# Performance work log

Hardware: AMD Instinct MI355X
Metric: run time of the kernel (lower is better)

Reference implementation:

```python
import jax, jax.numpy as jnp
import numpy as np

N = 20000      # nodes per graph
E = 320000     # edges per graph (before self-loops)
G = 256        # graphs (strings) per side
VOCAB = 128    # NUMBER_EMBEDDINGS
D_IN = 128
HID = 64
H = 4
D_OUT = 128
NEG_SLOPE = 0.2  # PyG GATConv leaky_relu slope


def _gat(x, edge_index, W, att_s, att_d, bias, concat):
    """PyG GATConv: gather -> per-edge logits -> segment softmax over dst -> scatter.
    x: [N, F_in], W: [F_in, H*C], att_s/att_d: [H, C], bias: [H*C] or [C].
    Self-loops are added (PyG default add_self_loops=True)."""
    n = x.shape[0]
    h, c = att_s.shape
    loops = jnp.arange(n)
    src = jnp.concatenate([edge_index[0], loops])  # message sources j
    dst = jnp.concatenate([edge_index[1], loops])  # message targets i
    xh = (x @ W).reshape(n, h, c)                  # [N,H,C]
    a_s = jnp.einsum('nhc,hc->nh', xh, att_s)      # [N,H]
    a_d = jnp.einsum('nhc,hc->nh', xh, att_d)
    logits = jax.nn.leaky_relu(a_s[src] + a_d[dst], NEG_SLOPE)  # [E',H]
    m = jax.ops.segment_max(logits, dst, num_segments=n)
    m = jnp.where(jnp.isfinite(m), m, 0.0)
    e = jnp.exp(logits - m[dst])
    z = jax.ops.segment_sum(e, dst, num_segments=n)
    alpha = e / (z[dst] + 1e-16)                   # [E',H]
    msg = xh[src] * alpha[:, :, None]              # [E',H,C]
    out = jax.ops.segment_sum(msg, dst, num_segments=n)  # [N,H,C]
    out = out.reshape(n, h * c) if concat else out.mean(axis=1)
    return out + bias


def _encode(xi, ei, batch, emb, W1, as1, ad1, b1, lw1, lb1,
            W2, as2, ad2, b2, lw2, lb2, W3, as3, ad3, b3, lw3, lb3):
    e = emb[xi]  # [N, D_IN]
    x = jax.nn.relu(_gat(e, ei, W1, as1, ad1, b1, True) + e @ lw1 + lb1)
    x = jax.nn.relu(_gat(x, ei, W2, as2, ad2, b2, True) + x @ lw2 + lb2)
    x = _gat(x, ei, W3, as3, ad3, b3, False) + x @ lw3 + lb3  # [N, D_OUT]
    s = jax.ops.segment_sum(x, batch, num_segments=G)
    cnt = jax.ops.segment_sum(jnp.ones((x.shape[0],), x.dtype), batch, num_segments=G)
    return s / jnp.maximum(cnt, 1.0)[:, None]  # global_mean_pool -> [G, D_OUT]


def setup_inputs() -> dict:
    key = jax.random.key(0)
    ks = jax.random.split(key, 32)
    hc = H * HID  # 256
    def nrm(k, shape, scale=0.05):
        return jax.random.normal(k, shape, dtype=jnp.float32) * scale
    inp = {
        'x_l': jax.random.randint(ks[0], (N,), 0, VOCAB),
        'edge_l': jax.random.randint(ks[1], (2, E), 0, N),
        'batch_l': jnp.sort(jax.random.randint(ks[2], (N,), 0, G)),
        'x_r': jax.random.randint(ks[3], (N,), 0, VOCAB),
        'edge_r': jax.random.randint(ks[4], (2, E), 0, N),
        'batch_r': jnp.sort(jax.random.randint(ks[5], (N,), 0, G)),
        'emb': nrm(ks[6], (VOCAB, D_IN), 1.0),
        'W1': nrm(ks[7], (D_IN, hc)), 'as1': nrm(ks[8], (H, HID)), 'ad1': nrm(ks[9], (H, HID)),
        'b1': jnp.zeros((hc,), jnp.float32), 'lw1': nrm(ks[10], (D_IN, hc)), 'lb1': jnp.zeros((hc,), jnp.float32),
        'W2': nrm(ks[11], (hc, hc)), 'as2': nrm(ks[12], (H, HID)), 'ad2': nrm(ks[13], (H, HID)),
        'b2': jnp.zeros((hc,), jnp.float32), 'lw2': nrm(ks[14], (hc, hc)), 'lb2': jnp.zeros((hc,), jnp.float32),
        'W3': nrm(ks[15], (hc, H * D_OUT)), 'as3': nrm(ks[16], (H, D_OUT)), 'ad3': nrm(ks[17], (H, D_OUT)),
        'b3': jnp.zeros((D_OUT,), jnp.float32), 'lw3': nrm(ks[18], (hc, D_OUT)), 'lb3': jnp.zeros((D_OUT,), jnp.float32),
    }
    return inp


def reference(x_l, edge_l, batch_l, x_r, edge_r, batch_r, emb,
              W1, as1, ad1, b1, lw1, lb1,
              W2, as2, ad2, b2, lw2, lb2,
              W3, as3, ad3, b3, lw3, lb3):
    params = (emb, W1, as1, ad1, b1, lw1, lb1, W2, as2, ad2, b2, lw2, lb2,
              W3, as3, ad3, b3, lw3, lb3)
    out_l = _encode(x_l, edge_l, batch_l, *params)
    out_r = _encode(x_r, edge_r, batch_r, *params)
    return (out_l, out_r)
```

## Files before the change

kernel.cpp:

```cpp
#include <hip/hip_runtime.h>

#define GG 256

typedef __bf16 bf16x8 __attribute__((ext_vector_type(8)));
typedef __bf16 bf16x4 __attribute__((ext_vector_type(4)));
typedef float floatx4 __attribute__((ext_vector_type(4)));
typedef float f32x2 __attribute__((ext_vector_type(2)));

__device__ __forceinline__ float lrelu(float x) { return x > 0.f ? x : 0.2f * x; }

__device__ __forceinline__ int permM(int m) {
    int g = m >> 6, q = m & 63;
    return (g << 6) | ((q & 3) << 4) | (q >> 2);
}

__device__ __forceinline__ void wt1(const float* __restrict__ B, __bf16* __restrict__ Bt,
                                    int K, int M, int idx) {
    int k = idx / M, m = idx - k * M;
    Bt[(size_t)permM(m) * K + k] = (__bf16)B[idx];
}
__device__ __forceinline__ void wattn1(const float* __restrict__ W,
                                       const float* __restrict__ as_,
                                       const float* __restrict__ ad_,
                                       __bf16* __restrict__ dst, int K, int C, int idx) {
    int j = idx / K, k = idx - j * K;
    float v = 0.f;
    if (j < 8) {
        int h = j & 3;
        const float* att = (j < 4) ? as_ : ad_;
        int M = 4 * C;
        for (int c = 0; c < C; c++) v += W[(size_t)k * M + h * C + c] * att[h * C + c];
    }
    dst[(size_t)j * K + k] = (__bf16)v;
}

__global__ void k_wprep(const float* W1, const float* lw1, const float* as1, const float* ad1,
                        const float* W2, const float* lw2, const float* as2, const float* ad2,
                        const float* W3, const float* lw3, const float* as3, const float* ad3,
                        __bf16* B1t, __bf16* B2t, __bf16* B3t) {
    int idx = blockIdx.x * blockDim.x + threadIdx.x;
    if (idx < 32768) { wt1(W1, B1t, 128, 256, idx); return; }
    idx -= 32768;
    if (idx < 32768) { wt1(lw1, B1t + 256 * 128, 128, 256, idx); return; }
    idx -= 32768;
    if (idx < 2048) { wattn1(W1, as1, ad1, B1t + 512 * 128, 128, 64, idx); return; }
    idx -= 2048;
    if (idx < 65536) { wt1(W2, B2t, 256, 256, idx); return; }
    idx -= 65536;
    if (idx < 65536) { wt1(lw2, B2t + 256 * 256, 256, 256, idx); return; }
    idx -= 65536;
    if (idx < 4096) { wattn1(W2, as2, ad2, B2t + 512 * 256, 256, 64, idx); return; }
    idx -= 4096;
    if (idx < 131072) { wt1(W3, B3t, 256, 512, idx); return; }
    idx -= 131072;
    if (idx < 32768) { wt1(lw3, B3t + 512 * 256, 256, 128, idx); return; }
    idx -= 32768;
    if (idx < 4096) { wattn1(W3, as3, ad3, B3t + 640 * 256, 256, 128, idx); return; }
}

template <int K, bool EMB, bool LINBF>
__global__ __launch_bounds__(256) void k_gemm_all(const __bf16* __restrict__ A,
                                                  const int* __restrict__ xl,
                                                  const int* __restrict__ xr,
                                                  const float* __restrict__ emb,
                                                  const __bf16* __restrict__ Bt,
                                                  int n, int n1, int Mx, int Ml,
                                                  unsigned char* __restrict__ x8, int ldx,
                                                  float* __restrict__ linf,
                                                  __bf16* __restrict__ linb, int ldl,
                                                  const float* __restrict__ bias1,
                                                  const float* __restrict__ bias2,
                                                  float* __restrict__ a_s,
                                                  float* __restrict__ a_d) {
    constexpr int KS = K / 32;
    constexpr int LDK = K + 8;
    constexpr int LPR = K / 8;
    constexpr int NCH = 64 * LPR / 256;
    __shared__ __bf16 S[64 * LDK];
    int tid = threadIdx.x;
    int wave = tid >> 6, lane = tid & 63;
    int row0 = blockIdx.x * 64;
#pragma unroll
    for (int c = 0; c < NCH; c++) {
        int i = tid + c * 256;
        int r = i / LPR, ko = (i - r * LPR) * 8;
        int gr = row0 + r;
        bf16x8 v = {};
        if (gr < n) {
            if (EMB) {
                int xi = (gr < n1) ? xl[gr] : xr[gr - n1];
                const float4* src = (const float4*)(emb + ((size_t)xi << 7) + ko);
                float4 q0 = src[0], q1 = src[1];
                v = bf16x8{(__bf16)q0.x, (__bf16)q0.y, (__bf16)q0.z, (__bf16)q0.w,
                           (__bf16)q1.x, (__bf16)q1.y, (__bf16)q1.z, (__bf16)q1.w};
            } else {
                v = *(const bf16x8*)(A + (size_t)gr * K + ko);
            }
        }
        *(bf16x8*)&S[r * LDK + ko] = v;
    }
    __syncthreads();
    int kOff = (lane >> 4) * 8;
    int colBase = lane & 15;
    bf16x8 af[KS];
#pragma unroll
    for (int ks = 0; ks < KS; ks++)
        af[ks] = *(const bf16x8*)&S[(wave * 16 + colBase) * LDK + ks * 32 + kOff];
    int Mtot = Mx + Ml;
    int gr0 = row0 + wave * 16 + ((lane >> 4) << 2);
    int half = (Mtot / 128) * 64;
    int c0beg = blockIdx.y * half;
    int T = half / 64;
    bf16x8 regs[NCH];
#pragma unroll
    for (int c = 0; c < NCH; c++) {
        int i = tid + c * 256;
        int r = i / LPR, ko = (i - r * LPR) * 8;
        regs[c] = *(const bf16x8*)(Bt + (size_t)(c0beg + r) * K + ko);
    }
    for (int t = 0; t < T; t++) {
        __syncthreads();
#pragma unroll
        for (int c = 0; c < NCH; c++) {
            int i = tid + c * 256;
            int r = i / LPR, ko = (i - r * LPR) * 8;
            *(bf16x8*)&S[r * LDK + ko] = regs[c];
        }
        if (t + 1 < T) {
            int c0n = c0beg + (t + 1) * 64;
#pragma unroll
            for (int c = 0; c < NCH; c++) {
                int i = tid + c * 256;
                int r = i / LPR, ko = (i - r * LPR) * 8;
                regs[c] = *(const bf16x8*)(Bt + (size_t)(c0n + r) * K + ko);
            }
        }
        __syncthreads();
        floatx4 acc[4] = {};
#pragma unroll
        for (int ct = 0; ct < 4; ct++) {
#pragma unroll
            for (int ks = 0; ks < KS; ks++) {
                bf16x8 bf = *(const bf16x8*)&S[(ct * 16 + colBase) * LDK + ks * 32 + kOff];
                acc[ct] = __builtin_amdgcn_mfma_f32_16x16x32_bf16(af[ks], bf, acc[ct], 0, 0, 0);
            }
        }
        int c0 = c0beg + t * 64;
        if (c0 < Mx) {
#pragma unroll
            for (int r = 0; r < 4; r++) {
                int gr = gr0 + r;
                if (gr >= n) continue;
                int p = __builtin_amdgcn_cvt_pk_fp8_f32(acc[0][r], acc[1][r], 0, false);
                p = __builtin_amdgcn_cvt_pk_fp8_f32(acc[2][r], acc[3][r], p, true);
                *(unsigned int*)(x8 + (size_t)gr * ldx + c0 + colBase * 4) = (unsigned int)p;
            }
        } else {
            int c2 = c0 + colBase * 4 - Mx;
#pragma unroll
            for (int r = 0; r < 4; r++) {
                int gr = gr0 + r;
                if (gr >= n) continue;
                float v0 = acc[0][r] + bias1[c2 + 0];
                float v1 = acc[1][r] + bias1[c2 + 1];
                float v2 = acc[2][r] + bias1[c2 + 2];
                float v3 = acc[3][r] + bias1[c2 + 3];
                if (bias2) {
                    v0 += bias2[c2 + 0]; v1 += bias2[c2 + 1];
                    v2 += bias2[c2 + 2]; v3 += bias2[c2 + 3];
                }
                if (LINBF) {
                    bf16x4 o = {(__bf16)v0, (__bf16)v1, (__bf16)v2, (__bf16)v3};
                    *(bf16x4*)(linb + (size_t)gr * ldl + c2) = o;
                } else {
                    float4 o = {v0, v1, v2, v3};
                    *(float4*)(linf + (size_t)gr * ldl + c2) = o;
                }
            }
        }
    }
    if (blockIdx.y == 1) {
        floatx4 acc = {};
        const __bf16* bp = Bt + (size_t)(Mtot + colBase) * K + kOff;
#pragma unroll
        for (int ks = 0; ks < KS; ks++) {
            bf16x8 bf = *(const bf16x8*)(bp + ks * 32);
            acc = __builtin_amdgcn_mfma_f32_16x16x32_bf16(af[ks], bf, acc, 0, 0, 0);
        }
        if (colBase < 8) {
            float* dst = (colBase < 4) ? a_s : a_d;
            int h = colBase & 3;
#pragma unroll
            for (int r = 0; r < 4; r++) {
                int gr = gr0 + r;
                if (gr < n) dst[gr * 4 + h] = acc[r];
            }
        }
    }
}

__global__ void k_hist2(const int* __restrict__ el, const int* __restrict__ er,
                        int E, int n, int* __restrict__ deg) {
    int e = blockIdx.x * blockDim.x + threadIdx.x;
    if (e >= 2 * E) return;
    int d = (e < E) ? el[E + e] : er[E + (e - E)] + n;
    atomicAdd(&deg[d], 1);
}

__global__ __launch_bounds__(1024) void k_scan1(int* __restrict__ rp, int n,
                                                int* __restrict__ part) {
    __shared__ int wsum[16];
    int i = blockIdx.x * 1024 + threadIdx.x;
    int lane = threadIdx.x & 63, wid = threadIdx.x >> 6;
    int v = (i < n) ? rp[i] : 0;
    int inc = v;
#pragma unroll
    for (int off = 1; off < 64; off <<= 1) {
        int t = __shfl_up(inc, off, 64);
        if (lane >= off) inc += t;
    }
    if (lane == 63) wsum[wid] = inc;
    __syncthreads();
    if (wid == 0) {
        int wv = (lane < 16) ? wsum[lane] : 0;
        int winc = wv;
#pragma unroll
        for (int off = 1; off < 16; off <<= 1) {
            int t = __shfl_up(winc, off, 64);
            if (lane >= off) winc += t;
        }
        if (lane < 16) wsum[lane] = winc - wv;
        if (lane == 15) part[blockIdx.x] = winc;
    }
    __syncthreads();
    if (i < n) rp[i] = wsum[wid] + (inc - v);
}

__global__ void k_scan2(int* __restrict__ part, int nb) {
    int lane = threadIdx.x;
    int v = (lane < nb) ? part[lane] : 0;
    int inc = v;
#pragma unroll
    for (int off = 1; off < 64; off <<= 1) {
        int t = __shfl_up(inc, off, 64);
        if (lane >= off) inc += t;
    }
    if (lane < nb) part[lane] = inc - v;
}

__global__ __launch_bounds__(1024) void k_scan3(int* __restrict__ rp, int n,
                                                const int* __restrict__ part) {
    int i = blockIdx.x * 1024 + threadIdx.x;
    if (i < n) rp[i] += part[blockIdx.x];
}

__global__ void k_fill2(const int* __restrict__ el, const int* __restrict__ er,
                        int E, int n, int* __restrict__ rp, int* __restrict__ csr) {
    int e = blockIdx.x * blockDim.x + threadIdx.x;
    if (e >= 2 * E) return;
    int d, s;
    if (e < E) { s = el[e]; d = el[E + e]; }
    else       { s = er[e - E] + n; d = er[E + (e - E)] + n; }
    int pos = atomicAdd(&rp[d], 1);
    csr[pos] = s;
}

__device__ __forceinline__ void dec4(unsigned int u, float* f) {
    f32x2 a = __builtin_amdgcn_cvt_pk_f32_fp8(u, false);
    f32x2 b = __builtin_amdgcn_cvt_pk_f32_fp8(u, true);
    f[0] = a[0]; f[1] = a[1]; f[2] = b[0]; f[3] = b[1];
}

__global__ __launch_bounds__(256) void k_agg12(const int* __restrict__ rp,
                                               const int* __restrict__ csr,
                                               const float* __restrict__ a_s,
                                               const float* __restrict__ a_d,
                                               const unsigned char* __restrict__ x8,
                                               const __bf16* __restrict__ lin,
                                               __bf16* __restrict__ out_bf, int n) {
    int wv = (int)((blockIdx.x * blockDim.x + threadIdx.x) >> 6);
    int lane = threadIdx.x & 63;
    int sub = lane >> 5, sl = lane & 31;
    int node = wv * 2 + sub;
    if (node >= n) return;
    int c0 = sl * 8;
    int h = sl >> 3;
    int start = node ? rp[node - 1] : 0;
    int end = rp[node];
    float ad = a_d[node * 4 + h];
    float z = __expf(lrelu(a_s[node * 4 + h] + ad));
    float acc[8];
    {
        uint2 u = *(const uint2*)(x8 + (size_t)node * 256 + c0);
        float f[8];
        dec4(u.x, f); dec4(u.y, f + 4);
#pragma unroll
        for (int j = 0; j < 8; j++) acc[j] = z * f[j];
    }
    uint2 u0 = {}, u1 = {}, u2 = {};
    float A0 = 0.f, A1 = 0.f, A2 = 0.f;
    if (start < end) {
        int s = csr[start];
        u0 = *(const uint2*)(x8 + (size_t)s * 256 + c0);
        A0 = a_s[s * 4 + h];
    }
    if (start + 1 < end) {
        int s = csr[start + 1];
        u1 = *(const uint2*)(x8 + (size_t)s * 256 + c0);
        A1 = a_s[s * 4 + h];
    }
    if (start + 2 < end) {
        int s = csr[start + 2];
        u2 = *(const uint2*)(x8 + (size_t)s * 256 + c0);
        A2 = a_s[s * 4 + h];
    }
    for (int e = start; e < end; e++) {
        uint2 uc = u0;
        float ac = A0;
        u0 = u1; A0 = A1;
        u1 = u2; A1 = A2;
        if (e + 3 < end) {
            int s = csr[e + 3];
            u2 = *(const uint2*)(x8 + (size_t)s * 256 + c0);
            A2 = a_s[s * 4 + h];
        }
        float w = __expf(lrelu(ac + ad));
        z += w;
        float f[8];
        dec4(uc.x, f); dec4(uc.y, f + 4);
#pragma unroll
        for (int q = 0; q < 8; q++) acc[q] += w * f[q];
    }
    float inv = 1.f / (z + 1e-16f);
    bf16x8 l = *(const bf16x8*)(lin + (size_t)node * 256 + c0);
    bf16x8 r;
#pragma unroll
    for (int j = 0; j < 8; j++)
        r[j] = (__bf16)fmaxf(acc[j] * inv + (float)l[j], 0.f);
    *(bf16x8*)(out_bf + (size_t)node * 256 + c0) = r;
}

__global__ __launch_bounds__(256) void k_agg3(const int* __restrict__ rp,
                                              const int* __restrict__ csr,
                                              const float* __restrict__ a_s,
                                              const float* __restrict__ a_d,
                                              const unsigned int* __restrict__ x8,
                                              float* __restrict__ mean, int n) {
    int wv = (int)((blockIdx.x * blockDim.x + threadIdx.x) >> 6);
    int lane = threadIdx.x & 63;
    int sub = lane >> 5, sl = lane & 31;
    int node = wv * 2 + sub;
    if (node >= n) return;
    int h = sl >> 3;
    int start = node ? rp[node - 1] : 0;
    int end = rp[node];
    float ad = a_d[node * 4 + h];
    float z = __expf(lrelu(a_s[node * 4 + h] + ad));
    float acc[16];
    {
        uint4 u = *(const uint4*)(x8 + (size_t)node * 128 + sl * 4);
        float f[16];
        dec4(u.x, f); dec4(u.y, f + 4); dec4(u.z, f + 8); dec4(u.w, f + 12);
#pragma unroll
        for (int j = 0; j < 16; j++) acc[j] = z * f[j];
    }
    uint4 u0 = {}, u1 = {}, u2 = {};
    float A0 = 0.f, A1 = 0.f, A2 = 0.f;
    if (start < end) {
        int s = csr[start];
        u0 = *(const uint4*)(x8 + (size_t)s * 128 + sl * 4);
        A0 = a_s[s * 4 + h];
    }
    if (start + 1 < end) {
        int s = csr[start + 1];
        u1 = *(const uint4*)(x8 + (size_t)s * 128 + sl * 4);
        A1 = a_s[s * 4 + h];
    }
    if (start + 2 < end) {
        int s = csr[start + 2];
        u2 = *(const uint4*)(x8 + (size_t)s * 128 + sl * 4);
        A2 = a_s[s * 4 + h];
    }
    for (int e = start; e < end; e++) {
        uint4 uc = u0;
        float ac = A0;
        u0 = u1; A0 = A1;
        u1 = u2; A1 = A2;
        if (e + 3 < end) {
            int s = csr[e + 3];
            u2 = *(const uint4*)(x8 + (size_t)s * 128 + sl * 4);
            A2 = a_s[s * 4 + h];
        }
        float w = __expf(lrelu(ac + ad));
        z += w;
        float f[16];
        dec4(uc.x, f); dec4(uc.y, f + 4); dec4(uc.z, f + 8); dec4(uc.w, f + 12);
#pragma unroll
        for (int q = 0; q < 16; q++) acc[q] += w * f[q];
    }
    float scale = 0.25f / (z + 1e-16f);
#pragma unroll
    for (int j = 0; j < 16; j++) {
        float v = acc[j] * scale;
        v += __shfl_xor(v, 8, 64);
        v += __shfl_xor(v, 16, 64);
        acc[j] = v;
    }
    if ((sl & 24) == 0) {
        float4* op = (float4*)(mean + (size_t)node * 128 + sl * 16);
#pragma unroll
        for (int q = 0; q < 4; q++) {
            float4 o = {acc[4 * q], acc[4 * q + 1], acc[4 * q + 2], acc[4 * q + 3]};
            op[q] = o;
        }
    }
}

__global__ __launch_bounds__(128) void k_pool(const float* __restrict__ mean,
                                              const float* __restrict__ lin3,
                                              const float* __restrict__ b3,
                                              const int* __restrict__ bl,
                                              const int* __restrict__ br,
                                              int n, float* __restrict__ out) {
    int g = blockIdx.x, c = threadIdx.x;
    const int* b = (g < GG) ? bl : br;
    int tg = (g < GG) ? g : g - GG;
    int off = (g < GG) ? 0 : n;
    int s, e;
    { int lo = 0, hi = n; while (lo < hi) { int m = (lo + hi) >> 1; if (b[m] < tg) lo = m + 1; else hi = m; } s = lo; }
    { int lo = 0, hi = n; while (lo < hi) { int m = (lo + hi) >> 1; if (b[m] < tg + 1) lo = m + 1; else hi = m; } e = lo; }
    s += off; e += off;
    float acc = 0.f;
    for (int i = s; i < e; i++)
        acc += mean[(size_t)i * 128 + c] + lin3[(size_t)i * 128 + c];
    int cnt = e - s;
    out[(size_t)g * 128 + c] = cnt > 0 ? acc / (float)cnt + b3[c] : 0.f;
}

static inline int cdiv(int a, int b) { return (a + b - 1) / b; }

extern "C" void kernel_launch(void* const* d_in, const int* in_sizes, int n_in,
                              void* d_out, int out_size, void* d_ws, size_t ws_size,
                              hipStream_t stream) {
    const int* x_l = (const int*)d_in[0];
    const int* edge_l = (const int*)d_in[1];
    const int* batch_l = (const int*)d_in[2];
    const int* x_r = (const int*)d_in[3];
    const int* edge_r = (const int*)d_in[4];
    const int* batch_r = (const int*)d_in[5];
    const float* emb = (const float*)d_in[6];
    const float* W1 = (const float*)d_in[7];
    const float* as1 = (const float*)d_in[8];
    const float* ad1 = (const float*)d_in[9];
    const float* b1 = (const float*)d_in[10];
    const float* lw1 = (const float*)d_in[11];
    const float* lb1 = (const float*)d_in[12];
    const float* W2 = (const float*)d_in[13];
    const float* as2 = (const float*)d_in[14];
    const float* ad2 = (const float*)d_in[15];
    const float* b2 = (const float*)d_in[16];
    const float* lw2 = (const float*)d_in[17];
    const float* lb2 = (const float*)d_in[18];
    const float* W3 = (const float*)d_in[19];
    const float* as3 = (const float*)d_in[20];
    const float* ad3 = (const float*)d_in[21];
    const float* b3 = (const float*)d_in[22];
    const float* lw3 = (const float*)d_in[23];
    const float* lb3 = (const float*)d_in[24];

    const int n = in_sizes[0];
    const int E = in_sizes[1] / 2;
    const int N2 = 2 * n;
    const int NB = cdiv(N2, 1024);

    float* MEAN = (float*)d_ws;
    float* L3 = MEAN + (size_t)N2 * 128;
    float* a_s = L3 + (size_t)N2 * 128;
    float* a_d = a_s + (size_t)N2 * 4;
    int* rp = (int*)(a_d + (size_t)N2 * 4);
    int* csr = rp + N2;
    int* part = csr + 2 * E;
    __bf16* LINb = (__bf16*)(part + 64);
    unsigned char* X8a = (unsigned char*)(LINb + (size_t)N2 * 256);
    unsigned char* X8b = X8a + (size_t)N2 * 256;
    __bf16* Abf = (__bf16*)(X8b + (size_t)N2 * 512);
    __bf16* B1t = Abf + (size_t)N2 * 256;
    __bf16* B2t = B1t + 528 * 128;
    __bf16* B3t = B2t + 528 * 256;

    const int TB = 256;
    dim3 blk(TB);

    k_wprep<<<cdiv(370688, TB), blk, 0, stream>>>(W1, lw1, as1, ad1, W2, lw2, as2, ad2,
                                                  W3, lw3, as3, ad3, B1t, B2t, B3t);

    hipMemsetAsync(rp, 0, sizeof(int) * (size_t)N2, stream);
    k_hist2<<<cdiv(2 * E, TB), blk, 0, stream>>>(edge_l, edge_r, E, n, rp);
    k_scan1<<<NB, 1024, 0, stream>>>(rp, N2, part);
    k_scan2<<<1, 64, 0, stream>>>(part, NB);
    k_scan3<<<NB, 1024, 0, stream>>>(rp, N2, part);
    k_fill2<<<cdiv(2 * E, TB), blk, 0, stream>>>(edge_l, edge_r, E, n, rp, csr);

    k_gemm_all<128, true, true><<<dim3(cdiv(N2, 64), 2), blk, 0, stream>>>(
        nullptr, x_l, x_r, emb, B1t, N2, n, 256, 256, X8a, 256, nullptr, LINb, 256, lb1, b1, a_s, a_d);
    k_agg12<<<cdiv(N2, 8), blk, 0, stream>>>(rp, csr, a_s, a_d, X8a, LINb, Abf, N2);

    k_gemm_all<256, false, true><<<dim3(cdiv(N2, 64), 2), blk, 0, stream>>>(
        Abf, nullptr, nullptr, nullptr, B2t, N2, n, 256, 256, X8a, 256, nullptr, LINb, 256, lb2, b2, a_s, a_d);
    k_agg12<<<cdiv(N2, 8), blk, 0, stream>>>(rp, csr, a_s, a_d, X8a, LINb, Abf, N2);

    k_gemm_all<256, false, false><<<dim3(cdiv(N2, 64), 2), blk, 0, stream>>>(
        Abf, nullptr, nullptr, nullptr, B3t, N2, n, 512, 128, X8b, 512, L3, nullptr, 128, lb3, nullptr, a_s, a_d);
    k_agg3<<<cdiv(N2, 8), blk, 0, stream>>>(rp, csr, a_s, a_d, (const unsigned int*)X8b, MEAN, N2);
    k_pool<<<2 * GG, 128, 0, stream>>>(MEAN, L3, b3, batch_l, batch_r, n, (float*)d_out);
}
```

Measured before the change: 450.7 us.

## Reassociate layer-3 GEMM after aggregation and mean pooling

Layer 3 no longer runs a per-node 256x512 GEMM. The attention-weighted aggregation now works on the layer-2 output itself, stored as fp8 by agg12, and is pooled per graph into a small per-head buffer. The W3 and lw3 projections are then applied once per graph in a final small kernel. Attention logits come from a separate dot-product kernel. This cuts the large third GEMM and the wide x8 gather, at the cost of per-head accumulators (32 per lane), shared and global atomics, and extra fp8 quantization of the layer-2 activations.

Result: slower. 611.7 us (+35.7%).

```diff
diff --git a/kernel.cpp b/kernel.cpp
--- a/kernel.cpp
+++ b/kernel.cpp
@@ -37,7 +37,7 @@
 __global__ void k_wprep(const float* W1, const float* lw1, const float* as1, const float* ad1,
                         const float* W2, const float* lw2, const float* as2, const float* ad2,
                         const float* W3, const float* lw3, const float* as3, const float* ad3,
-                        __bf16* B1t, __bf16* B2t, __bf16* B3t) {
+                        __bf16* B1t, __bf16* B2t, __bf16* AT3, float* W3T, float* lw3T) {
     int idx = blockIdx.x * blockDim.x + threadIdx.x;
     if (idx < 32768) { wt1(W1, B1t, 128, 256, idx); return; }
     idx -= 32768;
@@ -51,11 +51,19 @@
     idx -= 65536;
     if (idx < 4096) { wattn1(W2, as2, ad2, B2t + 512 * 256, 256, 64, idx); return; }
     idx -= 4096;
-    if (idx < 131072) { wt1(W3, B3t, 256, 512, idx); return; }
+    if (idx < 131072) {
+        int m = idx >> 8, k = idx & 255;
+        W3T[(size_t)m * 256 + k] = W3[(size_t)k * 512 + m];
+        return;
+    }
     idx -= 131072;
-    if (idx < 32768) { wt1(lw3, B3t + 512 * 256, 256, 128, idx); return; }
+    if (idx < 32768) {
+        int c = idx >> 8, k = idx & 255;
+        lw3T[(size_t)c * 256 + k] = lw3[(size_t)k * 128 + c];
+        return;
+    }
     idx -= 32768;
-    if (idx < 4096) { wattn1(W3, as3, ad3, B3t + 640 * 256, 256, 128, idx); return; }
+    if (idx < 4096) { wattn1(W3, as3, ad3, AT3, 256, 128, idx); }
 }
 
 template <int K, bool EMB, bool LINBF>
@@ -271,13 +279,26 @@
     f[0] = a[0]; f[1] = a[1]; f[2] = b[0]; f[3] = b[1];
 }
 
+__global__ void k_cnt(const int* __restrict__ bl, const int* __restrict__ br,
+                      int n1, float* __restrict__ cinv) {
+    int g = threadIdx.x;
+    const int* b = (g < GG) ? bl : br;
+    int tg = (g < GG) ? g : g - GG;
+    int s, e;
+    { int lo = 0, hi = n1; while (lo < hi) { int m = (lo + hi) >> 1; if (b[m] < tg) lo = m + 1; else hi = m; } s = lo; }
+    { int lo = 0, hi = n1; while (lo < hi) { int m = (lo + hi) >> 1; if (b[m] < tg + 1) lo = m + 1; else hi = m; } e = lo; }
+    int cnt = e - s;
+    cinv[g] = cnt > 0 ? 1.f / (float)cnt : 0.f;
+}
+
 __global__ __launch_bounds__(256) void k_agg12(const int* __restrict__ rp,
                                                const int* __restrict__ csr,
                                                const float* __restrict__ a_s,
                                                const float* __restrict__ a_d,
                                                const unsigned char* __restrict__ x8,
                                                const __bf16* __restrict__ lin,
-                                               __bf16* __restrict__ out_bf, int n) {
+                                               __bf16* __restrict__ out_bf, int n,
+                                               unsigned char* __restrict__ x8o) {
     int wv = (int)((blockIdx.x * blockDim.x + threadIdx.x) >> 6);
     int lane = threadIdx.x & 63;
     int sub = lane >> 5, sl = lane & 31;
@@ -333,108 +354,223 @@
     }
     float inv = 1.f / (z + 1e-16f);
     bf16x8 l = *(const bf16x8*)(lin + (size_t)node * 256 + c0);
+    float rv[8];
+#pragma unroll
+    for (int j = 0; j < 8; j++)
+        rv[j] = fmaxf(acc[j] * inv + (float)l[j], 0.f);
     bf16x8 r;
 #pragma unroll
-    for (int j = 0; j < 8; j++)
-        r[j] = (__bf16)fmaxf(acc[j] * inv + (float)l[j], 0.f);
+    for (int j = 0; j < 8; j++) r[j] = (__bf16)rv[j];
     *(bf16x8*)(out_bf + (size_t)node * 256 + c0) = r;
-}
-
-__global__ __launch_bounds__(256) void k_agg3(const int* __restrict__ rp,
-                                              const int* __restrict__ csr,
-                                              const float* __restrict__ a_s,
-                                              const float* __restrict__ a_d,
-                                              const unsigned int* __restrict__ x8,
-                                              float* __restrict__ mean, int n) {
-    int wv = (int)((blockIdx.x * blockDim.x + threadIdx.x) >> 6);
-    int lane = threadIdx.x & 63;
-    int sub = lane >> 5, sl = lane & 31;
-    int node = wv * 2 + sub;
+    if (x8o) {
+        int p0 = __builtin_amdgcn_cvt_pk_fp8_f32(rv[0], rv[1], 0, false);
+        p0 = __builtin_amdgcn_cvt_pk_fp8_f32(rv[2], rv[3], p0, true);
+        int p1 = __builtin_amdgcn_cvt_pk_fp8_f32(rv[4], rv[5], 0, false);
+        p1 = __builtin_amdgcn_cvt_pk_fp8_f32(rv[6], rv[7], p1, true);
+        uint2 pv;
+        pv.x = (unsigned int)p0; pv.y = (unsigned int)p1;
+        *(uint2*)(x8o + (size_t)node * 256 + c0) = pv;
+    }
+}
+
+__global__ __launch_bounds__(256) void k_attn3(const __bf16* __restrict__ A,
+                                               const __bf16* __restrict__ T,
+                                               float* __restrict__ a_s,
+                                               float* __restrict__ a_d, int n) {
+    int idx = blockIdx.x * 256 + threadIdx.x;
+    int node = idx >> 3, j = idx & 7;
     if (node >= n) return;
-    int h = sl >> 3;
-    int start = node ? rp[node - 1] : 0;
-    int end = rp[node];
-    float ad = a_d[node * 4 + h];
-    float z = __expf(lrelu(a_s[node * 4 + h] + ad));
-    float acc[16];
-    {
-        uint4 u = *(const uint4*)(x8 + (size_t)node * 128 + sl * 4);
-        float f[16];
-        dec4(u.x, f); dec4(u.y, f + 4); dec4(u.z, f + 8); dec4(u.w, f + 12);
-#pragma unroll
-        for (int j = 0; j < 16; j++) acc[j] = z * f[j];
-    }
-    uint4 u0 = {}, u1 = {}, u2 = {};
-    float A0 = 0.f, A1 = 0.f, A2 = 0.f;
-    if (start < end) {
-        int s = csr[start];
-        u0 = *(const uint4*)(x8 + (size_t)s * 128 + sl * 4);
-        A0 = a_s[s * 4 + h];
-    }
-    if (start + 1 < end) {
-        int s = csr[start + 1];
-        u1 = *(const uint4*)(x8 + (size_t)s * 128 + sl * 4);
-        A1 = a_s[s * 4 + h];
-    }
-    if (start + 2 < end) {
-        int s = csr[start + 2];
-        u2 = *(const uint4*)(x8 + (size_t)s * 128 + sl * 4);
-        A2 = a_s[s * 4 + h];
-    }
-    for (int e = start; e < end; e++) {
-        uint4 uc = u0;
-        float ac = A0;
-        u0 = u1; A0 = A1;
-        u1 = u2; A1 = A2;
-        if (e + 3 < end) {
-            int s = csr[e + 3];
-            u2 = *(const uint4*)(x8 + (size_t)s * 128 + sl * 4);
-            A2 = a_s[s * 4 + h];
-        }
-        float w = __expf(lrelu(ac + ad));
-        z += w;
-        float f[16];
-        dec4(uc.x, f); dec4(uc.y, f + 4); dec4(uc.z, f + 8); dec4(uc.w, f + 12);
-#pragma unroll
-        for (int q = 0; q < 16; q++) acc[q] += w * f[q];
-    }
-    float scale = 0.25f / (z + 1e-16f);
-#pragma unroll
-    for (int j = 0; j < 16; j++) {
-        float v = acc[j] * scale;
-        v += __shfl_xor(v, 8, 64);
-        v += __shfl_xor(v, 16, 64);
-        acc[j] = v;
-    }
-    if ((sl & 24) == 0) {
-        float4* op = (float4*)(mean + (size_t)node * 128 + sl * 16);
-#pragma unroll
-        for (int q = 0; q < 4; q++) {
-            float4 o = {acc[4 * q], acc[4 * q + 1], acc[4 * q + 2], acc[4 * q + 3]};
-            op[q] = o;
-        }
-    }
-}
-
-__global__ __launch_bounds__(128) void k_pool(const float* __restrict__ mean,
-                                              const float* __restrict__ lin3,
-                                              const float* __restrict__ b3,
-                                              const int* __restrict__ bl,
-                                              const int* __restrict__ br,
-                                              int n, float* __restrict__ out) {
+    const __bf16* ar = A + (size_t)node * 256;
+    const __bf16* tr = T + j * 256;
+    float acc = 0.f;
+#pragma unroll
+    for (int k = 0; k < 256; k += 8) {
+        bf16x8 av = *(const bf16x8*)(ar + k);
+        bf16x8 tv = *(const bf16x8*)(tr + k);
+#pragma unroll
+        for (int q = 0; q < 8; q++) acc += (float)av[q] * (float)tv[q];
+    }
+    float* dst = (j < 4) ? a_s : a_d;
+    dst[(size_t)node * 4 + (j & 3)] = acc;
+}
+
+__global__ __launch_bounds__(256) void k_poolx(const __bf16* __restrict__ A,
+                                               const int* __restrict__ bl,
+                                               const int* __restrict__ br,
+                                               const float* __restrict__ cinv,
+                                               int n1, float* __restrict__ PX) {
     int g = blockIdx.x, c = threadIdx.x;
     const int* b = (g < GG) ? bl : br;
     int tg = (g < GG) ? g : g - GG;
-    int off = (g < GG) ? 0 : n;
+    int off = (g < GG) ? 0 : n1;
     int s, e;
-    { int lo = 0, hi = n; while (lo < hi) { int m = (lo + hi) >> 1; if (b[m] < tg) lo = m + 1; else hi = m; } s = lo; }
-    { int lo = 0, hi = n; while (lo < hi) { int m = (lo + hi) >> 1; if (b[m] < tg + 1) lo = m + 1; else hi = m; } e = lo; }
-    s += off; e += off;
+    { int lo = 0, hi = n1; while (lo < hi) { int m = (lo + hi) >> 1; if (b[m] < tg) lo = m + 1; else hi = m; } s = lo; }
+    { int lo = 0, hi = n1; while (lo < hi) { int m = (lo + hi) >> 1; if (b[m] < tg + 1) lo = m + 1; else hi = m; } e = lo; }
     float acc = 0.f;
-    for (int i = s; i < e; i++)
-        acc += mean[(size_t)i * 128 + c] + lin3[(size_t)i * 128 + c];
-    int cnt = e - s;
-    out[(size_t)g * 128 + c] = cnt > 0 ? acc / (float)cnt + b3[c] : 0.f;
+    for (int i = s; i < e; i++) acc += (float)A[((size_t)(off + i)) * 256 + c];
+    PX[(size_t)g * 256 + c] = acc * cinv[g];
+}
+
+__global__ __launch_bounds__(256) void k_agg3p(const int* __restrict__ rp,
+                                               const int* __restrict__ csr,
+                                               const float* __restrict__ a_s,
+                                               const float* __restrict__ a_d,
+                                               const unsigned char* __restrict__ x8,
+                                               const int* __restrict__ bl,
+                                               const int* __restrict__ br,
+                                               const float* __restrict__ cinv,
+                                               float* __restrict__ P, int n1) {
+    __shared__ float Pb[1024];
+    int tid = threadIdx.x;
+    int g = blockIdx.x >> 2, q = blockIdx.x & 3;
+    for (int i = tid; i < 1024; i += 256) Pb[i] = 0.f;
+    const int* b = (g < GG) ? bl : br;
+    int tg = (g < GG) ? g : g - GG;
+    int off = (g < GG) ? 0 : n1;
+    int s, e;
+    { int lo = 0, hi = n1; while (lo < hi) { int m = (lo + hi) >> 1; if (b[m] < tg) lo = m + 1; else hi = m; } s = lo; }
+    { int lo = 0, hi = n1; while (lo < hi) { int m = (lo + hi) >> 1; if (b[m] < tg + 1) lo = m + 1; else hi = m; } e = lo; }
+    int len = e - s;
+    int sq = s + ((len * q) >> 2), eq = s + ((len * (q + 1)) >> 2);
+    float ci = cinv[g] * 0.25f;
+    int lane = tid & 63, wvl = tid >> 6;
+    int sub = lane >> 5, sl = lane & 31;
+    __syncthreads();
+    for (int b0 = sq + wvl * 2; b0 < eq; b0 += 8) {
+        int nd = b0 + sub;
+        bool act = nd < eq;
+        int gn = off + (act ? nd : sq);
+        int start = gn ? rp[gn - 1] : 0;
+        int end = rp[gn];
+        float4 asv = *(const float4*)(a_s + (size_t)gn * 4);
+        float4 adv = *(const float4*)(a_d + (size_t)gn * 4);
+        float z[4], acc[32];
+        {
+            uint2 su = *(const uint2*)(x8 + (size_t)gn * 256 + sl * 8);
+            float f[8];
+            dec4(su.x, f); dec4(su.y, f + 4);
+            float w0 = __expf(lrelu(asv.x + adv.x)); z[0] = w0;
+            float w1 = __expf(lrelu(asv.y + adv.y)); z[1] = w1;
+            float w2 = __expf(lrelu(asv.z + adv.z)); z[2] = w2;
+            float w3 = __expf(lrelu(asv.w + adv.w)); z[3] = w3;
+#pragma unroll
+            for (int j = 0; j < 8; j++) {
+                acc[j] = w0 * f[j];
+                acc[8 + j] = w1 * f[j];
+                acc[16 + j] = w2 * f[j];
+                acc[24 + j] = w3 * f[j];
+            }
+        }
+        uint2 u0 = {}, u1 = {}, u2 = {};
+        float4 A0 = {}, A1 = {}, A2 = {};
+        if (start < end) {
+            int sv = csr[start];
+            u0 = *(const uint2*)(x8 + (size_t)sv * 256 + sl * 8);
+            A0 = *(const float4*)(a_s + (size_t)sv * 4);
+        }
+        if (start + 1 < end) {
+            int sv = csr[start + 1];
+            u1 = *(const uint2*)(x8 + (size_t)sv * 256 + sl * 8);
+            A1 = *(const float4*)(a_s + (size_t)sv * 4);
+        }
+        if (start + 2 < end) {
+            int sv = csr[start + 2];
+            u2 = *(const uint2*)(x8 + (size_t)sv * 256 + sl * 8);
+            A2 = *(const float4*)(a_s + (size_t)sv * 4);
+        }
+        for (int eI = start; eI < end; eI++) {
+            uint2 uc = u0;
+            float4 ac = A0;
+            u0 = u1; A0 = A1;
+            u1 = u2; A1 = A2;
+            if (eI + 3 < end) {
+                int sv = csr[eI + 3];
+                u2 = *(const uint2*)(x8 + (size_t)sv * 256 + sl * 8);
+                A2 = *(const float4*)(a_s + (size_t)sv * 4);
+            }
+            float f[8];
+            dec4(uc.x, f); dec4(uc.y, f + 4);
+            float w0 = __expf(lrelu(ac.x + adv.x)); z[0] += w0;
+            float w1 = __expf(lrelu(ac.y + adv.y)); z[1] += w1;
+            float w2 = __expf(lrelu(ac.z + adv.z)); z[2] += w2;
+            float w3 = __expf(lrelu(ac.w + adv.w)); z[3] += w3;
+#pragma unroll
+            for (int j = 0; j < 8; j++) {
+                acc[j] += w0 * f[j];
+                acc[8 + j] += w1 * f[j];
+                acc[16 + j] += w2 * f[j];
+                acc[24 + j] += w3 * f[j];
+            }
+        }
+#pragma unroll
+        for (int h = 0; h < 4; h++) {
+            float sc = act ? ci / (z[h] + 1e-16f) : 0.f;
+#pragma unroll
+            for (int j = 0; j < 8; j++) {
+                float v = acc[h * 8 + j] * sc;
+                v += __shfl_xor(v, 32);
+                if (sub == 0) atomicAdd(&Pb[h * 256 + j * 32 + sl], v);
+            }
+        }
+    }
+    __syncthreads();
+    for (int i = tid; i < 1024; i += 256) {
+        int h = i >> 8, r = i & 255, j = r >> 5, slx = r & 31;
+        atomicAdd(&P[(size_t)g * 1024 + h * 256 + slx * 8 + j], Pb[i]);
+    }
+}
+
+__global__ __launch_bounds__(256) void k_fin(const float* __restrict__ P,
+                                             const float* __restrict__ PX,
+                                             const float* __restrict__ W3T,
+                                             const float* __restrict__ lw3T,
+                                             const float* __restrict__ b3,
+                                             const float* __restrict__ lb3,
+                                             const float* __restrict__ cinv,
+                                             float* __restrict__ out) {
+    __shared__ float Ps[4][1024];
+    __shared__ float PXs[4][256];
+    int g0 = blockIdx.x * 4;
+    int tid = threadIdx.x;
+    for (int i = tid; i < 4096; i += 256)
+        Ps[i >> 10][i & 1023] = P[(size_t)g0 * 1024 + i];
+    for (int i = tid; i < 1024; i += 256)
+        PXs[i >> 8][i & 255] = PX[(size_t)g0 * 256 + i];
+    __syncthreads();
+    int c = tid & 127, gq = tid >> 7;
+    int ga = gq * 2, gb = ga + 1;
+    float acc0 = 0.f, acc1 = 0.f;
+#pragma unroll
+    for (int h = 0; h < 4; h++) {
+        const float4* wr = (const float4*)(W3T + ((size_t)(h * 128 + c)) * 256);
+        const float* pa = &Ps[ga][h * 256];
+        const float* pb = &Ps[gb][h * 256];
+#pragma unroll 4
+        for (int k = 0; k < 64; k++) {
+            float4 w = wr[k];
+            float4 va = *(const float4*)(pa + k * 4);
+            float4 vb = *(const float4*)(pb + k * 4);
+            acc0 += va.x * w.x + va.y * w.y + va.z * w.z + va.w * w.w;
+            acc1 += vb.x * w.x + vb.y * w.y + vb.z * w.z + vb.w * w.w;
+        }
+    }
+    {
+        const float4* wr = (const float4*)(lw3T + (size_t)c * 256);
+        const float* pa = &PXs[ga][0];
+        const float* pb = &PXs[gb][0];
+#pragma unroll 4
+        for (int k = 0; k < 64; k++) {
+            float4 w = wr[k];
+            float4 va = *(const float4*)(pa + k * 4);
+            float4 vb = *(const float4*)(pb + k * 4);
+            acc0 += va.x * w.x + va.y * w.y + va.z * w.z + va.w * w.w;
+            acc1 += vb.x * w.x + vb.y * w.y + vb.z * w.z + vb.w * w.w;
+        }
+    }
+    float bb = b3[c] + lb3[c];
+    int gA = g0 + ga, gB = g0 + gb;
+    out[(size_t)gA * 128 + c] = cinv[gA] > 0.f ? acc0 + bb : 0.f;
+    out[(size_t)gB * 128 + c] = cinv[gB] > 0.f ? acc1 + bb : 0.f;
 }
 
 static inline int cdiv(int a, int b) { return (a + b - 1) / b; }
@@ -473,28 +609,33 @@
     const int N2 = 2 * n;
     const int NB = cdiv(N2, 1024);
 
-    float* MEAN = (float*)d_ws;
-    float* L3 = MEAN + (size_t)N2 * 128;
-    float* a_s = L3 + (size_t)N2 * 128;
+    float* P = (float*)d_ws;
+    float* PX = P + 512 * 1024;
+    float* W3T = PX + 512 * 256;
+    float* lw3T = W3T + 512 * 256;
+    float* cinv = lw3T + 128 * 256;
+    float* a_s = cinv + 512;
     float* a_d = a_s + (size_t)N2 * 4;
     int* rp = (int*)(a_d + (size_t)N2 * 4);
     int* csr = rp + N2;
     int* part = csr + 2 * E;
     __bf16* LINb = (__bf16*)(part + 64);
     unsigned char* X8a = (unsigned char*)(LINb + (size_t)N2 * 256);
-    unsigned char* X8b = X8a + (size_t)N2 * 256;
-    __bf16* Abf = (__bf16*)(X8b + (size_t)N2 * 512);
+    unsigned char* X8c = X8a + (size_t)N2 * 256;
+    __bf16* Abf = (__bf16*)(X8c + (size_t)N2 * 256);
     __bf16* B1t = Abf + (size_t)N2 * 256;
     __bf16* B2t = B1t + 528 * 128;
-    __bf16* B3t = B2t + 528 * 256;
+    __bf16* AT3 = B2t + 528 * 256;
 
     const int TB = 256;
     dim3 blk(TB);
 
     k_wprep<<<cdiv(370688, TB), blk, 0, stream>>>(W1, lw1, as1, ad1, W2, lw2, as2, ad2,
-                                                  W3, lw3, as3, ad3, B1t, B2t, B3t);
+                                                  W3, lw3, as3, ad3, B1t, B2t, AT3, W3T, lw3T);
 
     hipMemsetAsync(rp, 0, sizeof(int) * (size_t)N2, stream);
+    hipMemsetAsync(P, 0, sizeof(float) * 512 * 1024, stream);
+    k_cnt<<<1, 512, 0, stream>>>(batch_l, batch_r, n, cinv);
     k_hist2<<<cdiv(2 * E, TB), blk, 0, stream>>>(edge_l, edge_r, E, n, rp);
     k_scan1<<<NB, 1024, 0, stream>>>(rp, N2, part);
     k_scan2<<<1, 64, 0, stream>>>(part, NB);
@@ -503,14 +644,14 @@
 
     k_gemm_all<128, true, true><<<dim3(cdiv(N2, 64), 2), blk, 0, stream>>>(
         nullptr, x_l, x_r, emb, B1t, N2, n, 256, 256, X8a, 256, nullptr, LINb, 256, lb1, b1, a_s, a_d);
-    k_agg12<<<cdiv(N2, 8), blk, 0, stream>>>(rp, csr, a_s, a_d, X8a, LINb, Abf, N2);
+    k_agg12<<<cdiv(N2, 8), blk, 0, stream>>>(rp, csr, a_s, a_d, X8a, LINb, Abf, N2, nullptr);
 
     k_gemm_all<256, false, true><<<dim3(cdiv(N2, 64), 2), blk, 0, stream>>>(
         Abf, nullptr, nullptr, nullptr, B2t, N2, n, 256, 256, X8a, 256, nullptr, LINb, 256, lb2, b2, a_s, a_d);
-    k_agg12<<<cdiv(N2, 8), blk, 0, stream>>>(rp, csr, a_s, a_d, X8a, LINb, Abf, N2);
-
-    k_gemm_all<256, false, false><<<dim3(cdiv(N2, 64), 2), blk, 0, stream>>>(
-        Abf, nullptr, nullptr, nullptr, B3t, N2, n, 512, 128, X8b, 512, L3, nullptr, 128, lb3, nullptr, a_s, a_d);
-    k_agg3<<<cdiv(N2, 8), blk, 0, stream>>>(rp, csr, a_s, a_d, (const unsigned int*)X8b, MEAN, N2);
-    k_pool<<<2 * GG, 128, 0, stream>>>(MEAN, L3, b3, batch_l, batch_r, n, (float*)d_out);
-}
+    k_agg12<<<cdiv(N2, 8), blk, 0, stream>>>(rp, csr, a_s, a_d, X8a, LINb, Abf, N2, X8c);
+
+    k_attn3<<<cdiv(N2 * 8, TB), blk, 0, stream>>>(Abf, AT3, a_s, a_d, N2);
+    k_poolx<<<2 * GG, 256, 0, stream>>>(Abf, batch_l, batch_r, cinv, n, PX);
+    k_agg3p<<<2 * GG * 4, blk, 0, stream>>>(rp, csr, a_s, a_d, X8c, batch_l, batch_r, cinv, P, n);
+    k_fin<<<GG / 2, blk, 0, stream>>>(P, PX, W3T, lw3T, b3, lb3, cinv, (float*)d_out);
+}
```

## Sort CSR neighbor lists and swizzle aggregation block order for locality

Applied to the files above, without the earlier changes.

Adds a kernel that insertion-sorts each node's incoming source list after the CSR fill, so gathers in the aggregation kernels walk source rows in ascending order and the edge order no longer depends on atomic fill order. The aggregation kernels also remap block indices so that consecutive blocks interleave the left-graph and right-graph halves, which may spread cache and channel traffic more evenly. The cost is an extra kernel launch with serial per-thread sorting. Degree is around 16, so the sort should be cheap.

Result: slower. 495.6 us (+10.0%).

```diff
diff --git a/kernel.cpp b/kernel.cpp
--- a/kernel.cpp
+++ b/kernel.cpp
@@ -55,7 +55,7 @@
     idx -= 131072;
     if (idx < 32768) { wt1(lw3, B3t + 512 * 256, 256, 128, idx); return; }
     idx -= 32768;
-    if (idx < 4096) { wattn1(W3, as3, ad3, B3t + 640 * 256, 256, 128, idx); return; }
+    if (idx < 4096) { wattn1(W3, as3, ad3, B3t + 640 * 256, 256, 128, idx); }
 }
 
 template <int K, bool EMB, bool LINBF>
@@ -265,10 +265,47 @@
     csr[pos] = s;
 }
 
+__global__ __launch_bounds__(128) void k_sortcsr(const int* __restrict__ rp,
+                                                 int* __restrict__ csr, int n) {
+    __shared__ int buf[128 * 49];
+    int t = blockIdx.x * 128 + threadIdx.x;
+    if (t >= n) return;
+    int s = t ? rp[t - 1] : 0;
+    int e = rp[t];
+    int d = e - s;
+    if (d <= 1) return;
+    if (d > 48) {
+        for (int i = s + 1; i < e; i++) {
+            int v = csr[i];
+            int j = i - 1;
+            while (j >= s && csr[j] > v) { csr[j + 1] = csr[j]; j--; }
+            csr[j + 1] = v;
+        }
+        return;
+    }
+    int* b = &buf[threadIdx.x * 49];
+    for (int i = 0; i < d; i++) b[i] = csr[s + i];
+    for (int i = 1; i < d; i++) {
+        int v = b[i];
+        int j = i - 1;
+        while (j >= 0 && b[j] > v) { b[j + 1] = b[j]; j--; }
+        b[j + 1] = v;
+    }
+    for (int i = 0; i < d; i++) csr[s + i] = b[i];
+}
+
 __device__ __forceinline__ void dec4(unsigned int u, float* f) {
     f32x2 a = __builtin_amdgcn_cvt_pk_f32_fp8(u, false);
     f32x2 b = __builtin_amdgcn_cvt_pk_f32_fp8(u, true);
     f[0] = a[0]; f[1] = a[1]; f[2] = b[0]; f[3] = b[1];
+}
+
+__device__ __forceinline__ int swz_block(int bid, int nbx) {
+    if (nbx & 7) return bid;
+    int halfb = nbx >> 1;
+    int grp = bid >> 3, r = bid & 7;
+    int j = grp * 4 + (r & 3);
+    return (r < 4) ? j : halfb + j;
 }
 
 __global__ __launch_bounds__(256) void k_agg12(const int* __restrict__ rp,
@@ -278,10 +315,10 @@
                                                const unsigned char* __restrict__ x8,
                                                const __bf16* __restrict__ lin,
                                                __bf16* __restrict__ out_bf, int n) {
-    int wv = (int)((blockIdx.x * blockDim.x + threadIdx.x) >> 6);
+    int nb = swz_block(blockIdx.x, gridDim.x);
     int lane = threadIdx.x & 63;
     int sub = lane >> 5, sl = lane & 31;
-    int node = wv * 2 + sub;
+    int node = nb * 8 + ((threadIdx.x >> 6) << 1) + sub;
     if (node >= n) return;
     int c0 = sl * 8;
     int h = sl >> 3;
@@ -346,10 +383,10 @@
                                               const float* __restrict__ a_d,
                                               const unsigned int* __restrict__ x8,
                                               float* __restrict__ mean, int n) {
-    int wv = (int)((blockIdx.x * blockDim.x + threadIdx.x) >> 6);
+    int nb = swz_block(blockIdx.x, gridDim.x);
     int lane = threadIdx.x & 63;
     int sub = lane >> 5, sl = lane & 31;
-    int node = wv * 2 + sub;
+    int node = nb * 8 + ((threadIdx.x >> 6) << 1) + sub;
     if (node >= n) return;
     int h = sl >> 3;
     int start = node ? rp[node - 1] : 0;
@@ -500,6 +537,7 @@
     k_scan2<<<1, 64, 0, stream>>>(part, NB);
     k_scan3<<<NB, 1024, 0, stream>>>(rp, N2, part);
     k_fill2<<<cdiv(2 * E, TB), blk, 0, stream>>>(edge_l, edge_r, E, n, rp, csr);
+    k_sortcsr<<<cdiv(N2, 128), dim3(128), 0, stream>>>(rp, csr, N2);
 
     k_gemm_all<128, true, true><<<dim3(cdiv(N2, 64), 2), blk, 0, stream>>>(
         nullptr, x_l, x_r, emb, B1t, N2, n, 256, 256, X8a, 256, nullptr, LINb, 256, lb1, b1, a_s, a_d);
```

## Deepen gather prefetch ring and swizzle block-to-node mapping in aggregation kernels

Applied to the files above, without the earlier changes.

The edge-gather loops in both aggregation kernels move from a 3-deep rolling prefetch to a ring of 8 (layers 1-2) or 4 (layer 3) in-flight neighbor loads, with an unrolled inner loop. This keeps more memory requests outstanding to hide gather latency. Block indices are also remapped so consecutive launched blocks alternate between the two halves of the node range (left and right graphs), likely to spread load or cache traffic across XCDs. The deeper ring raises register pressure and may lower occupancy.

After: 453.5 us. Within noise of the previous version (+0.6%).

```diff
diff --git a/kernel.cpp b/kernel.cpp
--- a/kernel.cpp
+++ b/kernel.cpp
@@ -55,7 +55,7 @@
     idx -= 131072;
     if (idx < 32768) { wt1(lw3, B3t + 512 * 256, 256, 128, idx); return; }
     idx -= 32768;
-    if (idx < 4096) { wattn1(W3, as3, ad3, B3t + 640 * 256, 256, 128, idx); return; }
+    if (idx < 4096) { wattn1(W3, as3, ad3, B3t + 640 * 256, 256, 128, idx); }
 }
 
 template <int K, bool EMB, bool LINBF>
@@ -271,6 +271,14 @@
     f[0] = a[0]; f[1] = a[1]; f[2] = b[0]; f[3] = b[1];
 }
 
+__device__ __forceinline__ int swz_block(int bid, int nbx) {
+    if (nbx & 7) return bid;
+    int halfb = nbx >> 1;
+    int grp = bid >> 3, r = bid & 7;
+    int j = grp * 4 + (r & 3);
+    return (r < 4) ? j : halfb + j;
+}
+
 __global__ __launch_bounds__(256) void k_agg12(const int* __restrict__ rp,
                                                const int* __restrict__ csr,
                                                const float* __restrict__ a_s,
@@ -278,10 +286,10 @@
                                                const unsigned char* __restrict__ x8,
                                                const __bf16* __restrict__ lin,
                                                __bf16* __restrict__ out_bf, int n) {
-    int wv = (int)((blockIdx.x * blockDim.x + threadIdx.x) >> 6);
+    int nb = swz_block(blockIdx.x, gridDim.x);
     int lane = threadIdx.x & 63;
     int sub = lane >> 5, sl = lane & 31;
-    int node = wv * 2 + sub;
+    int node = nb * 8 + ((threadIdx.x >> 6) << 1) + sub;
     if (node >= n) return;
     int c0 = sl * 8;
     int h = sl >> 3;
@@ -297,39 +305,36 @@
 #pragma unroll
         for (int j = 0; j < 8; j++) acc[j] = z * f[j];
     }
-    uint2 u0 = {}, u1 = {}, u2 = {};
-    float A0 = 0.f, A1 = 0.f, A2 = 0.f;
-    if (start < end) {
-        int s = csr[start];
-        u0 = *(const uint2*)(x8 + (size_t)s * 256 + c0);
-        A0 = a_s[s * 4 + h];
-    }
-    if (start + 1 < end) {
-        int s = csr[start + 1];
-        u1 = *(const uint2*)(x8 + (size_t)s * 256 + c0);
-        A1 = a_s[s * 4 + h];
-    }
-    if (start + 2 < end) {
-        int s = csr[start + 2];
-        u2 = *(const uint2*)(x8 + (size_t)s * 256 + c0);
-        A2 = a_s[s * 4 + h];
-    }
-    for (int e = start; e < end; e++) {
-        uint2 uc = u0;
-        float ac = A0;
-        u0 = u1; A0 = A1;
-        u1 = u2; A1 = A2;
-        if (e + 3 < end) {
-            int s = csr[e + 3];
-            u2 = *(const uint2*)(x8 + (size_t)s * 256 + c0);
-            A2 = a_s[s * 4 + h];
-        }
-        float w = __expf(lrelu(ac + ad));
-        z += w;
-        float f[8];
-        dec4(uc.x, f); dec4(uc.y, f + 4);
-#pragma unroll
-        for (int q = 0; q < 8; q++) acc[q] += w * f[q];
+    constexpr int D = 8;
+    uint2 u[D] = {};
+    float A[D] = {};
+#pragma unroll
+    for (int j = 0; j < D; j++) {
+        if (start + j < end) {
+            int s = csr[start + j];
+            u[j] = *(const uint2*)(x8 + (size_t)s * 256 + c0);
+            A[j] = a_s[s * 4 + h];
+        }
+    }
+    for (int e = start; e < end; e += D) {
+#pragma unroll
+        for (int j = 0; j < D; j++) {
+            if (e + j >= end) break;
+            uint2 uc = u[j];
+            float ac = A[j];
+            int pn = e + j + D;
+            if (pn < end) {
+                int s = csr[pn];
+                u[j] = *(const uint2*)(x8 + (size_t)s * 256 + c0);
+                A[j] = a_s[s * 4 + h];
+            }
+            float w = __expf(lrelu(ac + ad));
+            z += w;
+            float f[8];
+            dec4(uc.x, f); dec4(uc.y, f + 4);
+#pragma unroll
+            for (int q = 0; q < 8; q++) acc[q] += w * f[q];
+        }
     }
     float inv = 1.f / (z + 1e-16f);
     bf16x8 l = *(const bf16x8*)(lin + (size_t)node * 256 + c0);
@@ -346,10 +351,10 @@
                                               const float* __restrict__ a_d,
                                               const unsigned int* __restrict__ x8,
                                               float* __restrict__ mean, int n) {
-    int wv = (int)((blockIdx.x * blockDim.x + threadIdx.x) >> 6);
+    int nb = swz_block(blockIdx.x, gridDim.x);
     int lane = threadIdx.x & 63;
     int sub = lane >> 5, sl = lane & 31;
-    int node = wv * 2 + sub;
+    int node = nb * 8 + ((threadIdx.x >> 6) << 1) + sub;
     if (node >= n) return;
     int h = sl >> 3;
     int start = node ? rp[node - 1] : 0;
@@ -364,39 +369,36 @@
 #pragma unroll
         for (int j = 0; j < 16; j++) acc[j] = z * f[j];
     }
-    uint4 u0 = {}, u1 = {}, u2 = {};
-    float A0 = 0.f, A1 = 0.f, A2 = 0.f;
-    if (start < end) {
-        int s = csr[start];
-        u0 = *(const uint4*)(x8 + (size_t)s * 128 + sl * 4);
-        A0 = a_s[s * 4 + h];
-    }
-    if (start + 1 < end) {
-        int s = csr[start + 1];
-        u1 = *(const uint4*)(x8 + (size_t)s * 128 + sl * 4);
-        A1 = a_s[s * 4 + h];
-    }
-    if (start + 2 < end) {
-        int s = csr[start + 2];
-        u2 = *(const uint4*)(x8 + (size_t)s * 128 + sl * 4);
-        A2 = a_s[s * 4 + h];
-    }
-    for (int e = start; e < end; e++) {
-        uint4 uc = u0;
-        float ac = A0;
-        u0 = u1; A0 = A1;
-        u1 = u2; A1 = A2;
-        if (e + 3 < end) {
-            int s = csr[e + 3];
-            u2 = *(const uint4*)(x8 + (size_t)s * 128 + sl * 4);
-            A2 = a_s[s * 4 + h];
-        }
-        float w = __expf(lrelu(ac + ad));
-        z += w;
-        float f[16];
-        dec4(uc.x, f); dec4(uc.y, f + 4); dec4(uc.z, f + 8); dec4(uc.w, f + 12);
-#pragma unroll
-        for (int q = 0; q < 16; q++) acc[q] += w * f[q];
+    constexpr int D = 4;
+    uint4 u[D] = {};
+    float A[D] = {};
+#pragma unroll
+    for (int j = 0; j < D; j++) {
+        if (start + j < end) {
+            int s = csr[start + j];
+            u[j] = *(const uint4*)(x8 + (size_t)s * 128 + sl * 4);
+            A[j] = a_s[s * 4 + h];
+        }
+    }
+    for (int e = start; e < end; e += D) {
+#pragma unroll
+        for (int j = 0; j < D; j++) {
+            if (e + j >= end) break;
+            uint4 uc = u[j];
+            float ac = A[j];
+            int pn = e + j + D;
+            if (pn < end) {
+                int s = csr[pn];
+                u[j] = *(const uint4*)(x8 + (size_t)s * 128 + sl * 4);
+                A[j] = a_s[s * 4 + h];
+            }
+            float w = __expf(lrelu(ac + ad));
+            z += w;
+            float f[16];
+            dec4(uc.x, f); dec4(uc.y, f + 4); dec4(uc.z, f + 8); dec4(uc.w, f + 12);
+#pragma unroll
+            for (int q = 0; q < 16; q++) acc[q] += w * f[q];
+        }
     }
     float scale = 0.25f / (z + 1e-16f);
 #pragma unroll
```
